# Optimization experiments

Hardware: AMD Instinct MI355X
Metric: run time of the kernel (lower is better)

## Reference

```python
import jax, jax.numpy as jnp
import numpy as np

B, N, Q = 4, 4096, 4096
K = 32                    # max_neighbors (k = min(max_neighbors, N))
NUM_ATOM_TYPES = 100
EMBED_DIM = 32
RBF_DIM = 16
CUTOFF = 5.0
RBF_GAMMA = 1.0 / max(CUTOFF / max(RBF_DIM, 1), 1e-6) ** 2  # 10.24
EPS = 1e-12


def setup_inputs() -> dict:
    key = jax.random.key(0)
    k1, k2, k3, k4, k5 = jax.random.split(key, 5)
    coords = jax.random.normal(k1, (B, N, 3), dtype=jnp.float32) * 10.0
    atom_types = jax.random.randint(k2, (B, N), 0, NUM_ATOM_TYPES)
    radii = jax.random.uniform(k3, (B, N), dtype=jnp.float32) + 0.5
    query_points = jax.random.normal(k4, (B, Q, 3), dtype=jnp.float32) * 10.0
    atom_mask = jnp.ones((B, N), dtype=bool)
    query_mask = jnp.ones((B, Q), dtype=bool)
    embed_table = jax.random.normal(k5, (NUM_ATOM_TYPES, EMBED_DIM), dtype=jnp.float32)
    rbf_centers = jnp.linspace(0.0, CUTOFF, RBF_DIM, dtype=jnp.float32)
    return {"coords": coords, "atom_types": atom_types, "radii": radii,
            "query_points": query_points, "atom_mask": atom_mask,
            "query_mask": query_mask, "embed_table": embed_table,
            "rbf_centers": rbf_centers}


def reference(coords, atom_types, radii, query_points, atom_mask, query_mask,
              embed_table, rbf_centers):
    b = coords.shape[0]
    # stable pairwise distances [B, Q, N]
    diff = query_points[:, :, None, :] - coords[:, None, :, :]
    dists = jnp.sqrt(jnp.sum(diff * diff, axis=-1) + EPS)
    masked_dists = jnp.where(atom_mask[:, None, :], dists, jnp.inf)
    # smallest-k via top_k on negated distances -> [B, Q, K]
    neg_vals, sorted_indices = jax.lax.top_k(-masked_dists, K)
    sorted_dists = -neg_vals

    bidx = jnp.arange(b)[:, None, None]                       # [B,1,1]
    neighbor_atom_mask = atom_mask[bidx, sorted_indices]      # [B,Q,K]
    neighbor_mask = neighbor_atom_mask & (sorted_dists <= CUTOFF) & query_mask[:, :, None]

    neighbor_coords = coords[bidx, sorted_indices]            # [B,Q,K,3]
    neighbor_radii = radii[bidx, sorted_indices][..., None]   # [B,Q,K,1]
    neighbor_types = atom_types[bidx, sorted_indices]         # [B,Q,K]
    neighbor_emb = embed_table[neighbor_types]                # [B,Q,K,E]

    rel_pos = query_points[:, :, None, :] - neighbor_coords   # [B,Q,K,3]
    rel_dist = sorted_dists[..., None]                        # [B,Q,K,1]
    rbf = jnp.exp(-RBF_GAMMA * (rel_dist - rbf_centers[None, None, None, :]) ** 2)

    features = jnp.concatenate([rel_pos, neighbor_radii, neighbor_emb, rbf, rel_dist], axis=-1)
    features = jnp.where(neighbor_mask[..., None], features, 0.0)

    safe_indices = jnp.where(neighbor_atom_mask, sorted_indices, -1)
    safe_dists = jnp.where(neighbor_mask, sorted_dists, 0.0)
    return features, neighbor_mask, safe_indices, safe_dists
```

## Files before the change

kernel.cpp:

```cpp
#include <hip/hip_runtime.h>
#include <stdint.h>

#define B_ 4
#define N_ 4096
#define Q_ 4096
#define K_ 32
#define E_ 32
#define R_ 16
#define F_ 53

static constexpr int QPB = 16;
static constexpr int THREADS = QPB * 64;
static constexpr int CAP = 208;
static constexpr int TILE = K_ * F_;
static constexpr int NSLOT = 4;
static constexpr int POOLB = (QPB * CAP * 8 > NSLOT * TILE * 4)
                           ? (QPB * CAP * 8) : (NSLOT * TILE * 4);

__device__ __forceinline__ unsigned int s2bits(float qx, float qy, float qz,
                                               float cx, float cy, float cz) {
    const float dx = __fsub_rn(qx, cx);
    const float dy = __fsub_rn(qy, cy);
    const float dz = __fsub_rn(qz, cz);
    return __float_as_uint(
        __fadd_rn(__fadd_rn(__fmul_rn(dx, dx), __fmul_rn(dy, dy)),
                  __fmul_rn(dz, dz)));
}

__device__ __forceinline__ void bitonic_sort64_u32(unsigned int& v, int lane) {
    #pragma unroll
    for (int k = 2; k <= 64; k <<= 1) {
        #pragma unroll
        for (int j = k >> 1; j > 0; j >>= 1) {
            unsigned int o = __shfl_xor(v, j);
            const bool asc = ((lane & k) == 0);
            const bool lower = ((lane & j) == 0);
            unsigned int mn = v < o ? v : o;
            unsigned int mx = v < o ? o : v;
            v = (lower == asc) ? mn : mx;
        }
    }
}

__device__ __forceinline__ void bitonic_sort64_u64(unsigned long long& v, int lane) {
    #pragma unroll
    for (int k = 2; k <= 64; k <<= 1) {
        #pragma unroll
        for (int j = k >> 1; j > 0; j >>= 1) {
            unsigned long long o = __shfl_xor(v, j);
            const bool asc = ((lane & k) == 0);
            const bool lower = ((lane & j) == 0);
            unsigned long long mn = v < o ? v : o;
            unsigned long long mx = v < o ? o : v;
            v = (lower == asc) ? mn : mx;
        }
    }
}

__device__ __forceinline__ void merge64_u64(unsigned long long& best,
                                            unsigned long long c, int lane) {
    unsigned long long rev = __shfl(c, 63 - lane);
    unsigned long long v = best < rev ? best : rev;
    #pragma unroll
    for (int j = 32; j > 0; j >>= 1) {
        unsigned long long o = __shfl_xor(v, j);
        const bool lower = ((lane & j) == 0);
        unsigned long long mn = v < o ? v : o;
        unsigned long long mx = v < o ? o : v;
        v = lower ? mn : mx;
    }
    best = v;
}

__global__ __launch_bounds__(THREADS, 8)
void lfb_kernel(const float* __restrict__ coords,
                const int* __restrict__ atom_types,
                const float* __restrict__ radii,
                const float* __restrict__ qpts,
                const int* __restrict__ atom_mask,
                const int* __restrict__ query_mask,
                const float* __restrict__ embed,
                const float* __restrict__ centers,
                float* __restrict__ out)
{
    __shared__ __align__(16) float sx[N_], sy[N_], sz[N_];
    __shared__ unsigned int smaskw[N_ / 32];
    __shared__ __align__(16) unsigned char pool[POOLB];

    const int tid  = threadIdx.x;
    const int lane = tid & 63;
    const int wv   = tid >> 6;
    const int bq0  = blockIdx.x * QPB;
    const int b    = bq0 / Q_;

    for (int i = tid; i < N_; i += THREADS) {
        const float* c = coords + (size_t)(b * N_ + i) * 3;
        const bool mv = atom_mask[b * N_ + i] != 0;
        sx[i] = mv ? c[0] : 1e30f;
        sy[i] = mv ? c[1] : 1e30f;
        sz[i] = mv ? c[2] : 1e30f;
        unsigned long long bm = __ballot(mv);
        if ((lane & 31) == 0)
            smaskw[i >> 5] = (unsigned int)((lane == 0) ? bm : (bm >> 32));
    }
    __syncthreads();

    const int bq = bq0 + wv;
    const float qx = qpts[(size_t)bq * 3 + 0];
    const float qy = qpts[(size_t)bq * 3 + 1];
    const float qz = qpts[(size_t)bq * 3 + 2];

    unsigned int mnb = 0xFFFFFFFFu;
    for (int i = 0; i < N_ / 256; ++i) {
        const int a0 = i * 256 + lane * 4;
        const float4 X = *(const float4*)&sx[a0];
        const float4 Y = *(const float4*)&sy[a0];
        const float4 Z = *(const float4*)&sz[a0];
        const unsigned int s0 = s2bits(qx, qy, qz, X.x, Y.x, Z.x);
        const unsigned int s1 = s2bits(qx, qy, qz, X.y, Y.y, Z.y);
        const unsigned int s2 = s2bits(qx, qy, qz, X.z, Y.z, Z.z);
        const unsigned int s3 = s2bits(qx, qy, qz, X.w, Y.w, Z.w);
        const unsigned int m01 = s0 < s1 ? s0 : s1;
        const unsigned int m23 = s2 < s3 ? s2 : s3;
        const unsigned int m = m01 < m23 ? m01 : m23;
        mnb = mnb < m ? mnb : m;
    }
    bitonic_sort64_u32(mnb, lane);
    const unsigned int Ts = __shfl(mnb, 31);
    const float dT = __fsqrt_rn(__fadd_rn(__uint_as_float(Ts), 1e-12f));
    const float u = __uint_as_float(__float_as_uint(dT) + 1);
    unsigned int ST = __float_as_uint(__fmul_rn(u, u)) + 2;
    ST = ST < Ts ? Ts : ST;

    unsigned long long* cbuf = reinterpret_cast<unsigned long long*>(pool) + wv * CAP;
    const unsigned long long lt = (1ull << lane) - 1ull;
    int cnt = 0;
    for (int i = 0; i < N_ / 256; ++i) {
        const int a0 = i * 256 + lane * 4;
        const float4 X = *(const float4*)&sx[a0];
        const float4 Y = *(const float4*)&sy[a0];
        const float4 Z = *(const float4*)&sz[a0];
        unsigned int sb[4];
        sb[0] = s2bits(qx, qy, qz, X.x, Y.x, Z.x);
        sb[1] = s2bits(qx, qy, qz, X.y, Y.y, Z.y);
        sb[2] = s2bits(qx, qy, qz, X.z, Y.z, Z.z);
        sb[3] = s2bits(qx, qy, qz, X.w, Y.w, Z.w);
        #pragma unroll
        for (int j = 0; j < 4; ++j) {
            const bool pass = sb[j] <= ST;
            const unsigned long long m = __ballot(pass);
            if (pass) {
                const int slot = cnt + __popcll(m & lt);
                if (slot < CAP)
                    cbuf[slot] = ((unsigned long long)sb[j] << 32)
                               | (unsigned int)(a0 + j);
            }
            cnt += __popcll(m);
        }
    }

    unsigned long long key;

    if (cnt <= CAP) {
        unsigned long long best;
        const int nch = (cnt + 63) >> 6;
        for (int c = 0; c < nch; ++c) {
            const int slot = c * 64 + lane;
            unsigned long long v = ~0ull;
            if (slot < cnt) {
                const unsigned long long raw = cbuf[slot];
                const float s = __uint_as_float((unsigned int)(raw >> 32));
                const float d = __fsqrt_rn(__fadd_rn(s, 1e-12f));
                v = ((unsigned long long)__float_as_uint(d) << 32)
                  | (unsigned int)(raw & 0xFFFFFFFFull);
            }
            bitonic_sort64_u64(v, lane);
            if (c == 0) best = v;
            else        merge64_u64(best, v, lane);
        }
        key = best;
    } else {
        key = ~0ull;
        for (int base = 0; base < N_; base += 64) {
            const int a = base + lane;
            const unsigned int sb = s2bits(qx, qy, qz, sx[a], sy[a], sz[a]);
            const float d = __fsqrt_rn(__fadd_rn(__uint_as_float(sb), 1e-12f));
            unsigned long long cand =
                ((unsigned long long)__float_as_uint(d) << 32) | (unsigned int)a;
            const unsigned long long T = __shfl(key, 31);
            unsigned long long m = __ballot(cand < T);
            while (m) {
                const int src = __ffsll(m) - 1;
                m &= m - 1;
                const unsigned long long nk = __shfl(cand, src);
                const unsigned long long up = __shfl_up(key, 1);
                if (lane < K_) {
                    const unsigned long long repl =
                        (lane == 0) ? nk : (up <= nk ? nk : up);
                    key = (key <= nk) ? key : repl;
                }
            }
        }
    }

    const size_t BQK = (size_t)B_ * Q_ * K_;
    float* out_feat = out;
    float* out_mask = out + BQK * (size_t)F_;
    float* out_idx  = out_mask + BQK;
    float* out_dist = out_idx + BQK;

    const bool qm = query_mask[bq] != 0;

    const float d_l  = __uint_as_float((unsigned int)(key >> 32));
    const int   id_l = (int)(key & 0xFFFFFFFFull);
    const bool  am_l = ((smaskw[(id_l & (N_ - 1)) >> 5] >> (id_l & 31)) & 1u) != 0;
    const bool  nm_l = am_l && (d_l <= 5.0f) && qm;

    if (lane < K_) {
        const size_t o = (size_t)bq * K_ + lane;
        out_mask[o] = nm_l ? 1.0f : 0.0f;
        out_idx[o]  = am_l ? (float)id_l : -1.0f;
        out_dist[o] = nm_l ? d_l : 0.0f;
    }

    __syncthreads();

    float* slot = reinterpret_cast<float*>(pool) + (wv & (NSLOT - 1)) * TILE;
    for (int r = 0; r < QPB / NSLOT; ++r) {
        if ((wv >> 2) == r) {
            if (lane < K_) {
                float* f = slot + lane * F_;
                f[0] = nm_l ? __fsub_rn(qx, sx[id_l]) : 0.0f;
                f[1] = nm_l ? __fsub_rn(qy, sy[id_l]) : 0.0f;
                f[2] = nm_l ? __fsub_rn(qz, sz[id_l]) : 0.0f;
                f[3] = nm_l ? radii[b * N_ + id_l] : 0.0f;

                const int t = atom_types[b * N_ + id_l];
                const float4* er4 = (const float4*)(embed + t * E_);
                #pragma unroll
                for (int e = 0; e < E_ / 4; ++e) {
                    const float4 v = er4[e];
                    f[4 + e * 4 + 0] = nm_l ? v.x : 0.0f;
                    f[4 + e * 4 + 1] = nm_l ? v.y : 0.0f;
                    f[4 + e * 4 + 2] = nm_l ? v.z : 0.0f;
                    f[4 + e * 4 + 3] = nm_l ? v.w : 0.0f;
                }

                const float NG = -(float)(256.0 / 25.0);
                #pragma unroll
                for (int rr = 0; rr < R_; ++rr) {
                    const float dd = __fsub_rn(d_l, centers[rr]);
                    const float a2 = __fmul_rn(dd, dd);
                    f[36 + rr] = nm_l ? expf(__fmul_rn(NG, a2)) : 0.0f;
                }
                f[52] = nm_l ? d_l : 0.0f;
            }
            const float4* s4 = (const float4*)slot;
            float4* d4 = (float4*)(out_feat + (size_t)bq * (size_t)TILE);
            for (int t4 = lane; t4 < TILE / 4; t4 += 64) d4[t4] = s4[t4];
        }
        __syncthreads();
    }
}

extern "C" void kernel_launch(void* const* d_in, const int* in_sizes, int n_in,
                              void* d_out, int out_size, void* d_ws, size_t ws_size,
                              hipStream_t stream) {
    const float* coords     = (const float*)d_in[0];
    const int*   atom_types = (const int*)d_in[1];
    const float* radii      = (const float*)d_in[2];
    const float* qpts       = (const float*)d_in[3];
    const int*   atom_mask  = (const int*)d_in[4];
    const int*   query_mask = (const int*)d_in[5];
    const float* embed      = (const float*)d_in[6];
    const float* centers    = (const float*)d_in[7];

    dim3 grid((B_ * Q_) / QPB);
    dim3 block(THREADS);
    lfb_kernel<<<grid, block, 0, stream>>>(coords, atom_types, radii, qpts,
                                           atom_mask, query_mask, embed, centers,
                                           (float*)d_out);
}
```

Before: 62.84 us.

## Process two queries per wave to halve per-query coordinate staging

Each block now handles 32 queries with 16 waves, so every wave computes distances for two queries from the same shared-memory coordinate loads. This halves the number of blocks that load the 4096-atom batch into LDS. Candidate compaction switches from ballot/popcount prefix slots to shared-memory atomicAdd counters, with per-query capacity reduced to 104. The atom-mask bitmap is replaced by an infinity check on the distance key. The extra register pressure, the atomic contention and the smaller capacity may trigger the slow fallback path more often.

```diff
diff --git a/kernel.cpp b/kernel.cpp
--- a/kernel.cpp
+++ b/kernel.cpp
@@ -9,13 +9,14 @@
 #define R_ 16
 #define F_ 53
 
-static constexpr int QPB = 16;
-static constexpr int THREADS = QPB * 64;
-static constexpr int CAP = 208;
-static constexpr int TILE = K_ * F_;
-static constexpr int NSLOT = 4;
-static constexpr int POOLB = (QPB * CAP * 8 > NSLOT * TILE * 4)
-                           ? (QPB * CAP * 8) : (NSLOT * TILE * 4);
+static constexpr int WAVES   = 16;
+static constexpr int THREADS = WAVES * 64;
+static constexpr int QPB     = 32;
+static constexpr int CAP     = 104;
+static constexpr int TILE    = K_ * F_;
+static constexpr int NSLOT   = 4;
+static constexpr int POOLB   = (QPB * CAP * 8 > NSLOT * TILE * 4)
+                             ? (QPB * CAP * 8) : (NSLOT * TILE * 4);
 
 __device__ __forceinline__ unsigned int s2bits(float qx, float qy, float qz,
                                                float cx, float cy, float cz) {
@@ -25,6 +26,13 @@
     return __float_as_uint(
         __fadd_rn(__fadd_rn(__fmul_rn(dx, dx), __fmul_rn(dy, dy)),
                   __fmul_rn(dz, dz)));
+}
+
+__device__ __forceinline__ unsigned int sbits_threshold(unsigned int Ts) {
+    const float dT = __fsqrt_rn(__fadd_rn(__uint_as_float(Ts), 1e-12f));
+    const float u  = __uint_as_float(__float_as_uint(dT) + 1);
+    unsigned int ST = __float_as_uint(__fmul_rn(u, u)) + 2;
+    return ST < Ts ? Ts : ST;
 }
 
 __device__ __forceinline__ void bitonic_sort64_u32(unsigned int& v, int lane) {
@@ -84,8 +92,8 @@
                 float* __restrict__ out)
 {
     __shared__ __align__(16) float sx[N_], sy[N_], sz[N_];
-    __shared__ unsigned int smaskw[N_ / 32];
     __shared__ __align__(16) unsigned char pool[POOLB];
+    __shared__ int wcnt[QPB];
 
     const int tid  = threadIdx.x;
     const int lane = tid & 63;
@@ -99,88 +107,107 @@
         sx[i] = mv ? c[0] : 1e30f;
         sy[i] = mv ? c[1] : 1e30f;
         sz[i] = mv ? c[2] : 1e30f;
-        unsigned long long bm = __ballot(mv);
-        if ((lane & 31) == 0)
-            smaskw[i >> 5] = (unsigned int)((lane == 0) ? bm : (bm >> 32));
-    }
+    }
+    if (tid < QPB) wcnt[tid] = 0;
     __syncthreads();
 
-    const int bq = bq0 + wv;
-    const float qx = qpts[(size_t)bq * 3 + 0];
-    const float qy = qpts[(size_t)bq * 3 + 1];
-    const float qz = qpts[(size_t)bq * 3 + 2];
-
-    unsigned int mnb = 0xFFFFFFFFu;
+    const int qA = bq0 + wv;
+    const int qB = bq0 + WAVES + wv;
+    const float qxA = qpts[(size_t)qA * 3 + 0];
+    const float qyA = qpts[(size_t)qA * 3 + 1];
+    const float qzA = qpts[(size_t)qA * 3 + 2];
+    const float qxB = qpts[(size_t)qB * 3 + 0];
+    const float qyB = qpts[(size_t)qB * 3 + 1];
+    const float qzB = qpts[(size_t)qB * 3 + 2];
+
+    unsigned int mnA = 0xFFFFFFFFu, mnB = 0xFFFFFFFFu;
     for (int i = 0; i < N_ / 256; ++i) {
         const int a0 = i * 256 + lane * 4;
         const float4 X = *(const float4*)&sx[a0];
         const float4 Y = *(const float4*)&sy[a0];
         const float4 Z = *(const float4*)&sz[a0];
-        const unsigned int s0 = s2bits(qx, qy, qz, X.x, Y.x, Z.x);
-        const unsigned int s1 = s2bits(qx, qy, qz, X.y, Y.y, Z.y);
-        const unsigned int s2 = s2bits(qx, qy, qz, X.z, Y.z, Z.z);
-        const unsigned int s3 = s2bits(qx, qy, qz, X.w, Y.w, Z.w);
-        const unsigned int m01 = s0 < s1 ? s0 : s1;
-        const unsigned int m23 = s2 < s3 ? s2 : s3;
-        const unsigned int m = m01 < m23 ? m01 : m23;
-        mnb = mnb < m ? mnb : m;
-    }
-    bitonic_sort64_u32(mnb, lane);
-    const unsigned int Ts = __shfl(mnb, 31);
-    const float dT = __fsqrt_rn(__fadd_rn(__uint_as_float(Ts), 1e-12f));
-    const float u = __uint_as_float(__float_as_uint(dT) + 1);
-    unsigned int ST = __float_as_uint(__fmul_rn(u, u)) + 2;
-    ST = ST < Ts ? Ts : ST;
-
-    unsigned long long* cbuf = reinterpret_cast<unsigned long long*>(pool) + wv * CAP;
-    const unsigned long long lt = (1ull << lane) - 1ull;
-    int cnt = 0;
+        unsigned int a0b = s2bits(qxA, qyA, qzA, X.x, Y.x, Z.x);
+        unsigned int a1b = s2bits(qxA, qyA, qzA, X.y, Y.y, Z.y);
+        unsigned int a2b = s2bits(qxA, qyA, qzA, X.z, Y.z, Z.z);
+        unsigned int a3b = s2bits(qxA, qyA, qzA, X.w, Y.w, Z.w);
+        unsigned int b0b = s2bits(qxB, qyB, qzB, X.x, Y.x, Z.x);
+        unsigned int b1b = s2bits(qxB, qyB, qzB, X.y, Y.y, Z.y);
+        unsigned int b2b = s2bits(qxB, qyB, qzB, X.z, Y.z, Z.z);
+        unsigned int b3b = s2bits(qxB, qyB, qzB, X.w, Y.w, Z.w);
+        unsigned int ma = (a0b < a1b ? a0b : a1b);
+        unsigned int mb = (a2b < a3b ? a2b : a3b);
+        ma = ma < mb ? ma : mb;
+        mnA = mnA < ma ? mnA : ma;
+        unsigned int na = (b0b < b1b ? b0b : b1b);
+        unsigned int nb = (b2b < b3b ? b2b : b3b);
+        na = na < nb ? na : nb;
+        mnB = mnB < na ? mnB : na;
+    }
+    bitonic_sort64_u32(mnA, lane);
+    bitonic_sort64_u32(mnB, lane);
+    const unsigned int STA = sbits_threshold(__shfl(mnA, 31));
+    const unsigned int STB = sbits_threshold(__shfl(mnB, 31));
+
+    unsigned long long* cb = reinterpret_cast<unsigned long long*>(pool);
+    unsigned long long* cbA = cb + (size_t)wv * CAP;
+    unsigned long long* cbB = cb + (size_t)(WAVES + wv) * CAP;
+    int* cntAp = &wcnt[wv];
+    int* cntBp = &wcnt[WAVES + wv];
     for (int i = 0; i < N_ / 256; ++i) {
         const int a0 = i * 256 + lane * 4;
         const float4 X = *(const float4*)&sx[a0];
         const float4 Y = *(const float4*)&sy[a0];
         const float4 Z = *(const float4*)&sz[a0];
-        unsigned int sb[4];
-        sb[0] = s2bits(qx, qy, qz, X.x, Y.x, Z.x);
-        sb[1] = s2bits(qx, qy, qz, X.y, Y.y, Z.y);
-        sb[2] = s2bits(qx, qy, qz, X.z, Y.z, Z.z);
-        sb[3] = s2bits(qx, qy, qz, X.w, Y.w, Z.w);
+        unsigned int sA[4], sB[4];
+        sA[0] = s2bits(qxA, qyA, qzA, X.x, Y.x, Z.x);
+        sA[1] = s2bits(qxA, qyA, qzA, X.y, Y.y, Z.y);
+        sA[2] = s2bits(qxA, qyA, qzA, X.z, Y.z, Z.z);
+        sA[3] = s2bits(qxA, qyA, qzA, X.w, Y.w, Z.w);
+        sB[0] = s2bits(qxB, qyB, qzB, X.x, Y.x, Z.x);
+        sB[1] = s2bits(qxB, qyB, qzB, X.y, Y.y, Z.y);
+        sB[2] = s2bits(qxB, qyB, qzB, X.z, Y.z, Z.z);
+        sB[3] = s2bits(qxB, qyB, qzB, X.w, Y.w, Z.w);
         #pragma unroll
         for (int j = 0; j < 4; ++j) {
-            const bool pass = sb[j] <= ST;
-            const unsigned long long m = __ballot(pass);
-            if (pass) {
-                const int slot = cnt + __popcll(m & lt);
+            if (sA[j] <= STA) {
+                const int slot = atomicAdd(cntAp, 1);
                 if (slot < CAP)
-                    cbuf[slot] = ((unsigned long long)sb[j] << 32)
-                               | (unsigned int)(a0 + j);
-            }
-            cnt += __popcll(m);
-        }
-    }
-
-    unsigned long long key;
-
-    if (cnt <= CAP) {
-        unsigned long long best;
-        const int nch = (cnt + 63) >> 6;
-        for (int c = 0; c < nch; ++c) {
-            const int slot = c * 64 + lane;
-            unsigned long long v = ~0ull;
-            if (slot < cnt) {
-                const unsigned long long raw = cbuf[slot];
-                const float s = __uint_as_float((unsigned int)(raw >> 32));
-                const float d = __fsqrt_rn(__fadd_rn(s, 1e-12f));
-                v = ((unsigned long long)__float_as_uint(d) << 32)
-                  | (unsigned int)(raw & 0xFFFFFFFFull);
-            }
-            bitonic_sort64_u64(v, lane);
-            if (c == 0) best = v;
-            else        merge64_u64(best, v, lane);
-        }
-        key = best;
-    } else {
-        key = ~0ull;
+                    cbA[slot] = ((unsigned long long)sA[j] << 32)
+                              | (unsigned int)(a0 + j);
+            }
+            if (sB[j] <= STB) {
+                const int slot = atomicAdd(cntBp, 1);
+                if (slot < CAP)
+                    cbB[slot] = ((unsigned long long)sB[j] << 32)
+                              | (unsigned int)(a0 + j);
+            }
+        }
+    }
+    const int cntA = *cntAp;
+    const int cntB = *cntBp;
+
+    auto select_top32 = [&](const unsigned long long* cbuf, int cnt,
+                            float qx, float qy, float qz) -> unsigned long long {
+        if (cnt <= CAP) {
+            unsigned long long best = ~0ull;
+            const int nch = (cnt + 63) >> 6;
+            for (int c = 0; c < nch; ++c) {
+                const int slot = c * 64 + lane;
+                unsigned long long v = ~0ull;
+                if (slot < cnt) {
+                    const unsigned long long raw = cbuf[slot];
+                    const float s = __uint_as_float((unsigned int)(raw >> 32));
+                    const float d = __fsqrt_rn(__fadd_rn(s, 1e-12f));
+                    v = ((unsigned long long)__float_as_uint(d) << 32)
+                      | (unsigned int)(raw & 0xFFFFFFFFull);
+                }
+                bitonic_sort64_u64(v, lane);
+                if (c == 0) best = v;
+                else        merge64_u64(best, v, lane);
+            }
+            return best;
+        }
+        unsigned long long key = ~0ull;
         for (int base = 0; base < N_; base += 64) {
             const int a = base + lane;
             const unsigned int sb = s2bits(qx, qy, qz, sx[a], sy[a], sz[a]);
@@ -201,7 +228,11 @@
                 }
             }
         }
-    }
+        return key;
+    };
+
+    const unsigned long long keyA = select_top32(cbA, cntA, qxA, qyA, qzA);
+    const unsigned long long keyB = select_top32(cbB, cntB, qxB, qyB, qzB);
 
     const size_t BQK = (size_t)B_ * Q_ * K_;
     float* out_feat = out;
@@ -209,55 +240,80 @@
     float* out_idx  = out_mask + BQK;
     float* out_dist = out_idx + BQK;
 
-    const bool qm = query_mask[bq] != 0;
-
-    const float d_l  = __uint_as_float((unsigned int)(key >> 32));
-    const int   id_l = (int)(key & 0xFFFFFFFFull);
-    const bool  am_l = ((smaskw[(id_l & (N_ - 1)) >> 5] >> (id_l & 31)) & 1u) != 0;
-    const bool  nm_l = am_l && (d_l <= 5.0f) && qm;
+    const bool qmA = query_mask[qA] != 0;
+    const bool qmB = query_mask[qB] != 0;
 
     if (lane < K_) {
-        const size_t o = (size_t)bq * K_ + lane;
-        out_mask[o] = nm_l ? 1.0f : 0.0f;
-        out_idx[o]  = am_l ? (float)id_l : -1.0f;
-        out_dist[o] = nm_l ? d_l : 0.0f;
+        {
+            const float d = __uint_as_float((unsigned int)(keyA >> 32));
+            const int  id = (int)(keyA & 0xFFFFFFFFull);
+            const bool am = ((unsigned int)(keyA >> 32)) < 0x7F800000u;
+            const bool nm = am && (d <= 5.0f) && qmA;
+            const size_t o = (size_t)qA * K_ + lane;
+            out_mask[o] = nm ? 1.0f : 0.0f;
+            out_idx[o]  = am ? (float)id : -1.0f;
+            out_dist[o] = nm ? d : 0.0f;
+        }
+        {
+            const float d = __uint_as_float((unsigned int)(keyB >> 32));
+            const int  id = (int)(keyB & 0xFFFFFFFFull);
+            const bool am = ((unsigned int)(keyB >> 32)) < 0x7F800000u;
+            const bool nm = am && (d <= 5.0f) && qmB;
+            const size_t o = (size_t)qB * K_ + lane;
+            out_mask[o] = nm ? 1.0f : 0.0f;
+            out_idx[o]  = am ? (float)id : -1.0f;
+            out_dist[o] = nm ? d : 0.0f;
+        }
     }
 
     __syncthreads();
 
-    float* slot = reinterpret_cast<float*>(pool) + (wv & (NSLOT - 1)) * TILE;
-    for (int r = 0; r < QPB / NSLOT; ++r) {
-        if ((wv >> 2) == r) {
-            if (lane < K_) {
-                float* f = slot + lane * F_;
-                f[0] = nm_l ? __fsub_rn(qx, sx[id_l]) : 0.0f;
-                f[1] = nm_l ? __fsub_rn(qy, sy[id_l]) : 0.0f;
-                f[2] = nm_l ? __fsub_rn(qz, sz[id_l]) : 0.0f;
-                f[3] = nm_l ? radii[b * N_ + id_l] : 0.0f;
-
-                const int t = atom_types[b * N_ + id_l];
-                const float4* er4 = (const float4*)(embed + t * E_);
-                #pragma unroll
-                for (int e = 0; e < E_ / 4; ++e) {
-                    const float4 v = er4[e];
-                    f[4 + e * 4 + 0] = nm_l ? v.x : 0.0f;
-                    f[4 + e * 4 + 1] = nm_l ? v.y : 0.0f;
-                    f[4 + e * 4 + 2] = nm_l ? v.z : 0.0f;
-                    f[4 + e * 4 + 3] = nm_l ? v.w : 0.0f;
-                }
-
-                const float NG = -(float)(256.0 / 25.0);
-                #pragma unroll
-                for (int rr = 0; rr < R_; ++rr) {
-                    const float dd = __fsub_rn(d_l, centers[rr]);
-                    const float a2 = __fmul_rn(dd, dd);
-                    f[36 + rr] = nm_l ? expf(__fmul_rn(NG, a2)) : 0.0f;
-                }
-                f[52] = nm_l ? d_l : 0.0f;
-            }
-            const float4* s4 = (const float4*)slot;
-            float4* d4 = (float4*)(out_feat + (size_t)bq * (size_t)TILE);
-            for (int t4 = lane; t4 < TILE / 4; t4 += 64) d4[t4] = s4[t4];
+    auto build_and_store = [&](int q, unsigned long long key,
+                               float qx, float qy, float qz, bool qm,
+                               float* slotp) {
+        const float d_l  = __uint_as_float((unsigned int)(key >> 32));
+        const int   id_l = (int)(key & 0xFFFFFFFFull) & (N_ - 1);
+        const bool  am_l = ((unsigned int)(key >> 32)) < 0x7F800000u;
+        const bool  nm_l = am_l && (d_l <= 5.0f) && qm;
+
+        if (lane < K_) {
+            float* f = slotp + lane * F_;
+            f[0] = nm_l ? __fsub_rn(qx, sx[id_l]) : 0.0f;
+            f[1] = nm_l ? __fsub_rn(qy, sy[id_l]) : 0.0f;
+            f[2] = nm_l ? __fsub_rn(qz, sz[id_l]) : 0.0f;
+            f[3] = nm_l ? radii[b * N_ + id_l] : 0.0f;
+
+            const int t = atom_types[b * N_ + id_l];
+            const float4* er4 = (const float4*)(embed + t * E_);
+            #pragma unroll
+            for (int e = 0; e < E_ / 4; ++e) {
+                const float4 v = er4[e];
+                f[4 + e * 4 + 0] = nm_l ? v.x : 0.0f;
+                f[4 + e * 4 + 1] = nm_l ? v.y : 0.0f;
+                f[4 + e * 4 + 2] = nm_l ? v.z : 0.0f;
+                f[4 + e * 4 + 3] = nm_l ? v.w : 0.0f;
+            }
+
+            const float NG = -(float)(256.0 / 25.0);
+            #pragma unroll
+            for (int rr = 0; rr < R_; ++rr) {
+                const float dd = __fsub_rn(d_l, centers[rr]);
+                const float a2 = __fmul_rn(dd, dd);
+                f[36 + rr] = nm_l ? expf(__fmul_rn(NG, a2)) : 0.0f;
+            }
+            f[52] = nm_l ? d_l : 0.0f;
+        }
+        const float4* s4 = (const float4*)slotp;
+        float4* d4 = (float4*)(out_feat + (size_t)q * (size_t)TILE);
+        for (int t4 = lane; t4 < TILE / 4; t4 += 64) d4[t4] = s4[t4];
+    };
+
+    float* stagef = reinterpret_cast<float*>(pool);
+    for (int r = 0; r < 8; ++r) {
+        if ((wv >> 2) == (r & 3)) {
+            float* slotp = stagef + (size_t)(wv & (NSLOT - 1)) * TILE;
+            if (r < 4) build_and_store(qA, keyA, qxA, qyA, qzA, qmA, slotp);
+            else       build_and_store(qB, keyB, qxB, qyB, qzB, qmB, slotp);
         }
         __syncthreads();
     }
```

Result: slower. 66.98 us (+6.6%).
